# Optimization experiments

Measured on AMD Instinct MI355X. Metric: run time of the kernel, lower is better.

## Reference

```python
import jax, jax.numpy as jnp
import numpy as np

DECAY = 0.99
EPS = 1e-05
COMMITMENT_COST = 1.0
N_EMBED = 1024
DIM = 128


def setup_inputs() -> dict:
    key = jax.random.key(0)
    k1, k2, k3 = jax.random.split(key, 3)
    inputs = jax.random.normal(k1, (16, 64, 64, DIM), dtype=jnp.float32)
    embed = jax.random.normal(k2, (DIM, N_EMBED), dtype=jnp.float32)
    cluster_size = jnp.zeros((N_EMBED,), dtype=jnp.float32)
    embed_avg = embed.copy()
    return {"inputs": inputs, "embed": embed, "cluster_size": cluster_size,
            "embed_avg": embed_avg}


def reference(inputs, embed, cluster_size, embed_avg):
    # flatten: [N, dim]
    flatten = inputs.reshape(-1, DIM)
    # squared L2 distance to each code: [N, n_embed]
    dist = (jnp.sum(flatten * flatten, axis=1, keepdims=True)
            - 2.0 * flatten @ embed
            + jnp.sum(embed * embed, axis=0, keepdims=True))
    embed_ind_flat = jnp.argmin(dist, axis=1)                    # [N]
    embed_ind = embed_ind_flat.reshape(inputs.shape[:-1])        # [B,H,W]
    # quantize = embedding lookup of codebook columns
    quantize = embed.T[embed_ind]                                # [B,H,W,dim]

    # --- training-mode EMA codebook update (no grad in original) ---
    ones = jnp.ones_like(embed_ind_flat, dtype=flatten.dtype)
    embed_onehot_sum = jax.ops.segment_sum(ones, embed_ind_flat,
                                           num_segments=N_EMBED)            # [n_embed]
    embed_sum = jax.ops.segment_sum(flatten, embed_ind_flat,
                                    num_segments=N_EMBED).T                 # [dim, n_embed]
    cluster_size_new = cluster_size * DECAY + (1.0 - DECAY) * embed_onehot_sum
    embed_avg_new = embed_avg * DECAY + (1.0 - DECAY) * embed_sum
    n = jnp.sum(cluster_size_new)
    cs = (cluster_size_new + EPS) / (n + N_EMBED * EPS) * n
    embed_new = embed_avg_new / cs[None, :]                      # [dim, n_embed]

    loss = jnp.mean((quantize - inputs) ** 2) * COMMITMENT_COST
    quantize_st = inputs + (quantize - inputs)  # straight-through (identity in fwd)
    return quantize_st, embed_ind, loss, embed_new, cluster_size_new, embed_avg_new
```

## Files before the change

### kernel.cpp

```cpp
#include <hip/hip_runtime.h>


#define N_ROWS 65536
#define DIM 128
#define NE 1024

typedef __attribute__((ext_vector_type(8))) short short8;
typedef __attribute__((ext_vector_type(16))) float f32x16;

#define WS_ESQ    0
#define WS_CNTI   1024
#define WS_LOSS   2048
#define WS_N      2049
#define WS_ESUM   4096
#define WS_EHI    (WS_ESUM + DIM*NE)
#define WS_ELO    (WS_EHI + 65536)
#define WS_ET     (WS_ELO + 65536)
#define WS_BUCKET (WS_ET + DIM*NE)
#define WS_OFF    (WS_BUCKET + N_ROWS)
#define WS_POS    (WS_OFF + 1024)
#define WS_ZERO_BYTES ((WS_ESUM + DIM*NE) * 4)

#define O_Q    0
#define O_IND  (N_ROWS*DIM)
#define O_LOSS (O_IND + N_ROWS)
#define O_ENEW (O_LOSS + 1)
#define O_CS   (O_ENEW + DIM*NE)
#define O_EAVG (O_CS + NE)

__device__ __forceinline__ unsigned short f2bf(float f) {
    unsigned u = __float_as_uint(f);
    unsigned r = (u + 0x7fffu + ((u >> 16) & 1u)) >> 16;
    return (unsigned short)r;
}
__device__ __forceinline__ float bf2f(unsigned short h) {
    return __uint_as_float(((unsigned)h) << 16);
}
__device__ __forceinline__ void stage16(const void* g, void* l) {
    __builtin_amdgcn_global_load_lds(
        (const __attribute__((address_space(1))) unsigned*)g,
        (__attribute__((address_space(3))) unsigned*)l, 16, 0, 0);
}

__global__ __launch_bounds__(256) void k_prep(const float* __restrict__ E,
                                              float* __restrict__ ws) {
    __shared__ float ls[64 * 129];
    __shared__ float part[4][64];
    const int tid = threadIdx.x, b = blockIdx.x;
    const int lane = tid & 63, wid = tid >> 6;

    float sq = 0.f;
    #pragma unroll
    for (int t = 0; t < 32; ++t) {
        int k = t * 4 + wid;
        float v = E[k * NE + b * 64 + lane];
        ls[lane * 129 + k] = v;
        sq += v * v;
    }
    part[wid][lane] = sq;
    __syncthreads();
    if (tid < 64)
        ws[WS_ESQ + b * 64 + tid] =
            part[0][tid] + part[1][tid] + part[2][tid] + part[3][tid];

    char* ehiB = (char*)(ws + WS_EHI);
    char* eloB = (char*)(ws + WS_ELO);
    #pragma unroll
    for (int t = 0; t < 4; ++t) {
        int i = tid + t * 256;
        int c = i >> 4, slot = i & 15;
        int k0 = (slot ^ (c & 15)) * 8;
        short8 hv, lv;
        #pragma unroll
        for (int e = 0; e < 8; ++e) {
            float v = ls[c * 129 + k0 + e];
            unsigned short h = f2bf(v);
            hv[e] = (short)h;
            lv[e] = (short)f2bf(v - bf2f(h));
        }
        *(short8*)(ehiB + (size_t)b * 16384 + i * 16) = hv;
        *(short8*)(eloB + (size_t)b * 16384 + i * 16) = lv;
    }
    float* et = ws + WS_ET;
    #pragma unroll
    for (int t = 0; t < 8; ++t) {
        int i = tid + t * 256;
        int c = i >> 5, k4 = (i & 31) * 4;
        float4 v;
        v.x = ls[c * 129 + k4 + 0];
        v.y = ls[c * 129 + k4 + 1];
        v.z = ls[c * 129 + k4 + 2];
        v.w = ls[c * 129 + k4 + 3];
        *(float4*)(et + (size_t)(b * 64 + c) * DIM + k4) = v;
    }
}

__global__ __launch_bounds__(256, 2) void k_main(const float* __restrict__ X,
                                                 float* __restrict__ ws,
                                                 float* __restrict__ out) {
    __shared__ __align__(16) char es[2][32768];
    __shared__ __align__(16) float esq_lds[NE];
    __shared__ int ind_sh[128];
    __shared__ float red2[4];

    const int tid = threadIdx.x;
    const int lane = tid & 63;
    const int wid = tid >> 6;
    const int col0 = lane & 31;
    const int hi = lane >> 5;
    const int rowBase = blockIdx.x * 128;

    const char* ehiB = (const char*)(ws + WS_EHI);
    const char* eloB = (const char*)(ws + WS_ELO);

    #pragma unroll
    for (int t = 0; t < 4; ++t) {
        int i = tid + t * 256;
        stage16(ehiB + i * 16, &es[0][i * 16]);
        stage16(eloB + i * 16, &es[0][16384 + i * 16]);
    }

    ((float4*)esq_lds)[tid] = ((const float4*)(ws + WS_ESQ))[tid];

    short8 ah[8], al[8];
    {
        const float* xr = X + (size_t)(rowBase + wid * 32 + col0) * DIM + hi * 8;
        #pragma unroll
        for (int ks = 0; ks < 8; ++ks) {
            float4 a = *(const float4*)(xr + ks * 16);
            float4 b = *(const float4*)(xr + ks * 16 + 4);
            float xv[8] = {a.x, a.y, a.z, a.w, b.x, b.y, b.z, b.w};
            short8 h, l;
            #pragma unroll
            for (int e = 0; e < 8; ++e) {
                unsigned short hh = f2bf(xv[e]);
                h[e] = (short)hh;
                l[e] = (short)f2bf(xv[e] - bf2f(hh));
            }
            ah[ks] = h;
            al[ks] = l;
        }
    }
    __syncthreads();

    float bd[16];
    int bi[16];
    #pragma unroll
    for (int s = 0; s < 16; ++s) { bd[s] = 1e30f; bi[s] = 0; }

    const int swz = (col0 & 15) << 4;
    const int coff = col0 * 256;
    const int khb = hi * 16;

    for (int c = 0; c < 16; ++c) {
        const int cur = c & 1;
        if (c < 15) {
            const char* hp = ehiB + (c + 1) * 16384;
            const char* lp = eloB + (c + 1) * 16384;
            #pragma unroll
            for (int t = 0; t < 4; ++t) {
                int i = tid + t * 256;
                stage16(hp + i * 16, &es[cur ^ 1][i * 16]);
                stage16(lp + i * 16, &es[cur ^ 1][16384 + i * 16]);
            }
        }

        f32x16 acc0, acc1;
        #pragma unroll
        for (int s = 0; s < 16; ++s) { acc0[s] = 0.f; acc1[s] = 0.f; }

        const char* hb = es[cur];
        #pragma unroll
        for (int ks = 0; ks < 8; ++ks) {
            int kb = (ks * 32 + khb) ^ swz;
            short8 bh0 = *(const short8*)(hb + coff + kb);
            short8 bl0 = *(const short8*)(hb + 16384 + coff + kb);
            short8 bh1 = *(const short8*)(hb + 8192 + coff + kb);
            short8 bl1 = *(const short8*)(hb + 24576 + coff + kb);
            acc0 = __builtin_amdgcn_mfma_f32_32x32x16_bf16(ah[ks], bl0, acc0, 0, 0, 0);
            acc0 = __builtin_amdgcn_mfma_f32_32x32x16_bf16(al[ks], bh0, acc0, 0, 0, 0);
            acc0 = __builtin_amdgcn_mfma_f32_32x32x16_bf16(ah[ks], bh0, acc0, 0, 0, 0);
            acc1 = __builtin_amdgcn_mfma_f32_32x32x16_bf16(ah[ks], bl1, acc1, 0, 0, 0);
            acc1 = __builtin_amdgcn_mfma_f32_32x32x16_bf16(al[ks], bh1, acc1, 0, 0, 0);
            acc1 = __builtin_amdgcn_mfma_f32_32x32x16_bf16(ah[ks], bh1, acc1, 0, 0, 0);
        }

        float e0 = esq_lds[c * 64 + col0];
        float e1 = esq_lds[c * 64 + 32 + col0];
        int c0 = c * 64 + col0, c1 = c * 64 + 32 + col0;
        #pragma unroll
        for (int r = 0; r < 16; ++r) {
            float s0 = e0 - 2.f * acc0[r];
            if (s0 < bd[r]) { bd[r] = s0; bi[r] = c0; }
            float s1 = e1 - 2.f * acc1[r];
            if (s1 < bd[r]) { bd[r] = s1; bi[r] = c1; }
        }
        __syncthreads();
    }

    #pragma unroll
    for (int r = 0; r < 16; ++r) {
        #pragma unroll
        for (int off = 1; off < 32; off <<= 1) {
            float od = __shfl_xor(bd[r], off, 64);
            int oi = __shfl_xor(bi[r], off, 64);
            if (od < bd[r] || (od == bd[r] && oi < bi[r])) { bd[r] = od; bi[r] = oi; }
        }
    }
    if (col0 == 0) {
        int* cnt = (int*)(ws + WS_CNTI);
        #pragma unroll
        for (int r = 0; r < 16; ++r) {
            int row = wid * 32 + (r & 3) + 8 * (r >> 2) + 4 * hi;
            int b = bi[r];
            ind_sh[row] = b;
            out[O_IND + rowBase + row] = (float)b;
            atomicAdd(&cnt[b], 1);
        }
    }
    __syncthreads();

    float lp = 0.f;
    {
        const float* et = ws + WS_ET;
        int rsub = tid >> 5;
        int d4 = (tid & 31) * 4;
        #pragma unroll
        for (int seg = 0; seg < 16; ++seg) {
            int row = seg * 8 + rsub;
            int j = ind_sh[row];
            float4 xv = *(const float4*)(X + (size_t)(rowBase + row) * DIM + d4);
            float4 qv = *(const float4*)(et + (size_t)j * DIM + d4);
            float4 st;
            st.x = xv.x + (qv.x - xv.x);
            st.y = xv.y + (qv.y - xv.y);
            st.z = xv.z + (qv.z - xv.z);
            st.w = xv.w + (qv.w - xv.w);
            *(float4*)(out + O_Q + (size_t)(rowBase + row) * DIM + d4) = st;
            float dx;
            dx = qv.x - xv.x; lp += dx * dx;
            dx = qv.y - xv.y; lp += dx * dx;
            dx = qv.z - xv.z; lp += dx * dx;
            dx = qv.w - xv.w; lp += dx * dx;
        }
    }
    #pragma unroll
    for (int off = 32; off; off >>= 1) lp += __shfl_down(lp, off, 64);
    if (lane == 0) red2[wid] = lp;
    __syncthreads();
    if (tid == 0) atomicAdd(ws + WS_LOSS, red2[0] + red2[1] + red2[2] + red2[3]);
}

__global__ __launch_bounds__(1024) void k_scan(const float* __restrict__ CS,
                                               float* __restrict__ ws,
                                               float* __restrict__ out) {
    __shared__ int wsum[16];
    __shared__ float fsum[16];
    int tid = threadIdx.x;
    int* cnt = (int*)(ws + WS_CNTI);
    int v = cnt[tid];
    float csn = 0.99f * CS[tid] + 0.01f * (float)v;
    out[O_CS + tid] = csn;
    float s = csn;
    #pragma unroll
    for (int off = 32; off; off >>= 1) s += __shfl_down(s, off, 64);
    int sc = v;
    #pragma unroll
    for (int d = 1; d < 64; d <<= 1) {
        int t = __shfl_up(sc, d, 64);
        if ((tid & 63) >= d) sc += t;
    }
    if ((tid & 63) == 0) fsum[tid >> 6] = s;
    if ((tid & 63) == 63) wsum[tid >> 6] = sc;
    __syncthreads();
    if (tid == 0) {
        int run = 0;
        float n = 0.f;
        for (int w = 0; w < 16; ++w) {
            int t = wsum[w]; wsum[w] = run; run += t;
            n += fsum[w];
        }
        ws[WS_N] = n;
        out[O_LOSS] = ws[WS_LOSS] * (1.0f / ((float)N_ROWS * (float)DIM));
    }
    __syncthreads();
    ((int*)(ws + WS_OFF))[tid] = sc - v + wsum[tid >> 6];
    ((int*)(ws + WS_POS))[tid] = 0;
}

__global__ __launch_bounds__(256) void k_scatter(const float* __restrict__ out,
                                                 float* __restrict__ ws) {
    int i = blockIdx.x * 256 + threadIdx.x;
    int j = (int)out[O_IND + i];
    int* pos = (int*)(ws + WS_POS);
    int slot = atomicAdd(&pos[j], 1);
    ((int*)(ws + WS_BUCKET))[((int*)(ws + WS_OFF))[j] + slot] = i;
}

__global__ __launch_bounds__(128) void k_segsum(const float* __restrict__ X,
                                                float* __restrict__ ws) {
    __shared__ int offL[1025];
    __shared__ int rs[64];
    const int tid = threadIdx.x;
    const int p0 = blockIdx.x * 64;
    const int* off = (const int*)(ws + WS_OFF);
    #pragma unroll
    for (int t = 0; t < 8; ++t) offL[tid + t * 128] = off[tid + t * 128];
    if (tid == 0) offL[1024] = N_ROWS;
    if (tid < 64) rs[tid] = ((const int*)(ws + WS_BUCKET))[p0 + tid];
    __syncthreads();

    int lo = 0, hi2 = 1023;
    while (lo < hi2) {
        int mid = (lo + hi2 + 1) >> 1;
        if (offL[mid] <= p0) lo = mid; else hi2 = mid - 1;
    }
    int j = lo;
    int bnd = offL[j + 1];
    float* esum = ws + WS_ESUM;
    float acc = 0.f;
    #pragma unroll 2
    for (int base = 0; base < 64; base += 8) {
        float v[8];
        #pragma unroll
        for (int u = 0; u < 8; ++u)
            v[u] = X[(size_t)rs[base + u] * DIM + tid];
        #pragma unroll
        for (int u = 0; u < 8; ++u) {
            int p = p0 + base + u;
            if (p >= bnd) {
                atomicAdd(&esum[tid * NE + j], acc);
                acc = 0.f;
                do { ++j; bnd = offL[j + 1]; } while (p >= bnd);
            }
            acc += v[u];
        }
    }
    atomicAdd(&esum[tid * NE + j], acc);
}

__global__ __launch_bounds__(256) void k_final(const float* __restrict__ CS,
                                               const float* __restrict__ EA,
                                               const float* __restrict__ ws,
                                               float* __restrict__ out) {
    int d = blockIdx.x >> 2;
    int j = (blockIdx.x & 3) * 256 + threadIdx.x;
    float nall = ws[WS_N];
    float csn = 0.99f * CS[j] + 0.01f * (float)((const int*)(ws + WS_CNTI))[j];
    float cs = (csn + 1e-5f) / (nall + (float)NE * 1e-5f) * nall;
    float ean = EA[(size_t)d * NE + j] * 0.99f + 0.01f * ws[WS_ESUM + (size_t)d * NE + j];
    out[O_EAVG + (size_t)d * NE + j] = ean;
    out[O_ENEW + (size_t)d * NE + j] = ean / cs;
}

extern "C" void kernel_launch(void* const* d_in, const int* in_sizes, int n_in,
                              void* d_out, int out_size, void* d_ws, size_t ws_size,
                              hipStream_t stream) {
    const float* X = (const float*)d_in[0];
    const float* E = (const float*)d_in[1];
    const float* CS = (const float*)d_in[2];
    const float* EA = (const float*)d_in[3];
    float* out = (float*)d_out;
    float* ws = (float*)d_ws;

    hipMemsetAsync(d_ws, 0, (size_t)WS_ZERO_BYTES, stream);
    k_prep   <<<dim3(16),           dim3(256),  0, stream>>>(E, ws);
    k_main   <<<dim3(N_ROWS / 128), dim3(256),  0, stream>>>(X, ws, out);
    k_scan   <<<dim3(1),            dim3(1024), 0, stream>>>(CS, ws, out);
    k_scatter<<<dim3(N_ROWS / 256), dim3(256),  0, stream>>>(out, ws);
    k_segsum <<<dim3(N_ROWS / 64),  dim3(128),  0, stream>>>(X, ws);
    k_final  <<<dim3(512),          dim3(256),  0, stream>>>(CS, EA, ws, out);
}
```

Baseline: 215.1 us.

## Drop codebook low-bf16 split and parallelize prep across dimension quarters

The distance GEMM now uses only the high bf16 part of the codebook (two MFMA terms per tile instead of three), which halves the LDS staging of codebook tiles and removes the lo-codebook workspace. The hi and lo products go into separate accumulators, so the MFMAs no longer form one serial dependency chain. k_prep is split into four blocks per 64-code group, one per quarter of the dimension, and the squared norms are combined with atomics. Leaving out the codebook low part lowers dot-product precision, which can flip argmin ties or near-ties relative to the fp32 reference.

```diff
diff --git a/kernel.cpp b/kernel.cpp
--- a/kernel.cpp
+++ b/kernel.cpp
@@ -14,8 +14,7 @@
 #define WS_N      2049
 #define WS_ESUM   4096
 #define WS_EHI    (WS_ESUM + DIM*NE)
-#define WS_ELO    (WS_EHI + 65536)
-#define WS_ET     (WS_ELO + 65536)
+#define WS_ET     (WS_EHI + 65536)
 #define WS_BUCKET (WS_ET + DIM*NE)
 #define WS_OFF    (WS_BUCKET + N_ROWS)
 #define WS_POS    (WS_OFF + 1024)
@@ -44,61 +43,54 @@
 
 __global__ __launch_bounds__(256) void k_prep(const float* __restrict__ E,
                                               float* __restrict__ ws) {
-    __shared__ float ls[64 * 129];
+    __shared__ float ls[64][33];
     __shared__ float part[4][64];
-    const int tid = threadIdx.x, b = blockIdx.x;
+    const int tid = threadIdx.x;
+    const int b = blockIdx.x >> 2, kq = blockIdx.x & 3;
     const int lane = tid & 63, wid = tid >> 6;
 
     float sq = 0.f;
     #pragma unroll
-    for (int t = 0; t < 32; ++t) {
-        int k = t * 4 + wid;
-        float v = E[k * NE + b * 64 + lane];
-        ls[lane * 129 + k] = v;
+    for (int t = 0; t < 8; ++t) {
+        int kk = t * 4 + wid;
+        float v = E[(kq * 32 + kk) * NE + b * 64 + lane];
+        ls[lane][kk] = v;
         sq += v * v;
     }
     part[wid][lane] = sq;
     __syncthreads();
     if (tid < 64)
-        ws[WS_ESQ + b * 64 + tid] =
-            part[0][tid] + part[1][tid] + part[2][tid] + part[3][tid];
-
-    char* ehiB = (char*)(ws + WS_EHI);
-    char* eloB = (char*)(ws + WS_ELO);
-    #pragma unroll
-    for (int t = 0; t < 4; ++t) {
+        atomicAdd(ws + WS_ESQ + b * 64 + tid,
+                  part[0][tid] + part[1][tid] + part[2][tid] + part[3][tid]);
+
+    {
+        int c = tid >> 2, u = tid & 3;
+        int kk8 = kq * 4 + u;
+        int slot = kk8 ^ (c & 15);
+        short8 hv;
+        #pragma unroll
+        for (int e = 0; e < 8; ++e)
+            hv[e] = (short)f2bf(ls[c][u * 8 + e]);
+        *(short8*)((char*)(ws + WS_EHI) + (size_t)b * 16384 + c * 256 + slot * 16) = hv;
+    }
+    float* et = ws + WS_ET;
+    #pragma unroll
+    for (int t = 0; t < 2; ++t) {
         int i = tid + t * 256;
-        int c = i >> 4, slot = i & 15;
-        int k0 = (slot ^ (c & 15)) * 8;
-        short8 hv, lv;
-        #pragma unroll
-        for (int e = 0; e < 8; ++e) {
-            float v = ls[c * 129 + k0 + e];
-            unsigned short h = f2bf(v);
-            hv[e] = (short)h;
-            lv[e] = (short)f2bf(v - bf2f(h));
-        }
-        *(short8*)(ehiB + (size_t)b * 16384 + i * 16) = hv;
-        *(short8*)(eloB + (size_t)b * 16384 + i * 16) = lv;
-    }
-    float* et = ws + WS_ET;
-    #pragma unroll
-    for (int t = 0; t < 8; ++t) {
-        int i = tid + t * 256;
-        int c = i >> 5, k4 = (i & 31) * 4;
+        int c = i >> 3, k4i = i & 7;
         float4 v;
-        v.x = ls[c * 129 + k4 + 0];
-        v.y = ls[c * 129 + k4 + 1];
-        v.z = ls[c * 129 + k4 + 2];
-        v.w = ls[c * 129 + k4 + 3];
-        *(float4*)(et + (size_t)(b * 64 + c) * DIM + k4) = v;
+        v.x = ls[c][k4i * 4 + 0];
+        v.y = ls[c][k4i * 4 + 1];
+        v.z = ls[c][k4i * 4 + 2];
+        v.w = ls[c][k4i * 4 + 3];
+        *(float4*)(et + (size_t)(b * 64 + c) * DIM + kq * 32 + k4i * 4) = v;
     }
 }
 
 __global__ __launch_bounds__(256, 2) void k_main(const float* __restrict__ X,
                                                  float* __restrict__ ws,
                                                  float* __restrict__ out) {
-    __shared__ __align__(16) char es[2][32768];
+    __shared__ __align__(16) char es[2][16384];
     __shared__ __align__(16) float esq_lds[NE];
     __shared__ int ind_sh[128];
     __shared__ float red2[4];
@@ -111,13 +103,11 @@
     const int rowBase = blockIdx.x * 128;
 
     const char* ehiB = (const char*)(ws + WS_EHI);
-    const char* eloB = (const char*)(ws + WS_ELO);
 
     #pragma unroll
     for (int t = 0; t < 4; ++t) {
         int i = tid + t * 256;
         stage16(ehiB + i * 16, &es[0][i * 16]);
-        stage16(eloB + i * 16, &es[0][16384 + i * 16]);
     }
 
     ((float4*)esq_lds)[tid] = ((const float4*)(ws + WS_ESQ))[tid];
@@ -156,33 +146,27 @@
         const int cur = c & 1;
         if (c < 15) {
             const char* hp = ehiB + (c + 1) * 16384;
-            const char* lp = eloB + (c + 1) * 16384;
             #pragma unroll
             for (int t = 0; t < 4; ++t) {
                 int i = tid + t * 256;
                 stage16(hp + i * 16, &es[cur ^ 1][i * 16]);
-                stage16(lp + i * 16, &es[cur ^ 1][16384 + i * 16]);
             }
         }
 
-        f32x16 acc0, acc1;
-        #pragma unroll
-        for (int s = 0; s < 16; ++s) { acc0[s] = 0.f; acc1[s] = 0.f; }
+        f32x16 h0, l0, h1, l1;
+        #pragma unroll
+        for (int s = 0; s < 16; ++s) { h0[s] = 0.f; l0[s] = 0.f; h1[s] = 0.f; l1[s] = 0.f; }
 
         const char* hb = es[cur];
         #pragma unroll
         for (int ks = 0; ks < 8; ++ks) {
             int kb = (ks * 32 + khb) ^ swz;
             short8 bh0 = *(const short8*)(hb + coff + kb);
-            short8 bl0 = *(const short8*)(hb + 16384 + coff + kb);
             short8 bh1 = *(const short8*)(hb + 8192 + coff + kb);
-            short8 bl1 = *(const short8*)(hb + 24576 + coff + kb);
-            acc0 = __builtin_amdgcn_mfma_f32_32x32x16_bf16(ah[ks], bl0, acc0, 0, 0, 0);
-            acc0 = __builtin_amdgcn_mfma_f32_32x32x16_bf16(al[ks], bh0, acc0, 0, 0, 0);
-            acc0 = __builtin_amdgcn_mfma_f32_32x32x16_bf16(ah[ks], bh0, acc0, 0, 0, 0);
-            acc1 = __builtin_amdgcn_mfma_f32_32x32x16_bf16(ah[ks], bl1, acc1, 0, 0, 0);
-            acc1 = __builtin_amdgcn_mfma_f32_32x32x16_bf16(al[ks], bh1, acc1, 0, 0, 0);
-            acc1 = __builtin_amdgcn_mfma_f32_32x32x16_bf16(ah[ks], bh1, acc1, 0, 0, 0);
+            h0 = __builtin_amdgcn_mfma_f32_32x32x16_bf16(ah[ks], bh0, h0, 0, 0, 0);
+            l0 = __builtin_amdgcn_mfma_f32_32x32x16_bf16(al[ks], bh0, l0, 0, 0, 0);
+            h1 = __builtin_amdgcn_mfma_f32_32x32x16_bf16(ah[ks], bh1, h1, 0, 0, 0);
+            l1 = __builtin_amdgcn_mfma_f32_32x32x16_bf16(al[ks], bh1, l1, 0, 0, 0);
         }
 
         float e0 = esq_lds[c * 64 + col0];
@@ -190,9 +174,9 @@
         int c0 = c * 64 + col0, c1 = c * 64 + 32 + col0;
         #pragma unroll
         for (int r = 0; r < 16; ++r) {
-            float s0 = e0 - 2.f * acc0[r];
+            float s0 = e0 - 2.f * (h0[r] + l0[r]);
             if (s0 < bd[r]) { bd[r] = s0; bi[r] = c0; }
-            float s1 = e1 - 2.f * acc1[r];
+            float s1 = e1 - 2.f * (h1[r] + l1[r]);
             if (s1 < bd[r]) { bd[r] = s1; bi[r] = c1; }
         }
         __syncthreads();
@@ -364,7 +348,7 @@
     float* ws = (float*)d_ws;
 
     hipMemsetAsync(d_ws, 0, (size_t)WS_ZERO_BYTES, stream);
-    k_prep   <<<dim3(16),           dim3(256),  0, stream>>>(E, ws);
+    k_prep   <<<dim3(64),           dim3(256),  0, stream>>>(E, ws);
     k_main   <<<dim3(N_ROWS / 128), dim3(256),  0, stream>>>(X, ws, out);
     k_scan   <<<dim3(1),            dim3(1024), 0, stream>>>(CS, ws, out);
     k_scatter<<<dim3(N_ROWS / 256), dim3(256),  0, stream>>>(out, ws);
```

Result: faster. 204.2 us (-5.1%).
